# Optimization experiments

Hardware: AMD Instinct MI355X
Metric: run time of the kernel (lower is better)

The kernel has to match this reference:

```python
import jax, jax.numpy as jnp
import numpy as np

# dims
B, A, CIN, CC = 512, 256, 7, 16          # batch, num_actions, input channels, conv channels
D, H, DH, E = 48, 8, 6, 512              # token_dimension, heads, head_dim, num_embeddings
S, T = 32, 32                            # num_input_tokens, num_output_tokens
AH = H * DH                              # 48
NL = 4                                   # attention layers
CONV_IN = A * CC                         # 4096
ENC = S * D                              # 1536
DEC_OUT = A * CIN                        # 1792
SCALE = float(np.sqrt(D))                # module uses sqrt(input_embedding_dim)
EPS = 1e-5


def _ln(x, g, b):
    m = jnp.mean(x, axis=-1, keepdims=True)
    v = jnp.var(x, axis=-1, keepdims=True)
    return (x - m) * jax.lax.rsqrt(v + EPS) * g + b


def setup_inputs() -> dict:
    key = jax.random.key(0)
    ks = iter(jax.random.split(key, 64))
    def rn(shape, s=0.05):
        return jax.random.normal(next(ks), shape, dtype=jnp.float32) * s
    inp = {}
    inp['x'] = jax.random.normal(next(ks), (B, A, CIN), dtype=jnp.float32)
    inp['u'] = jax.random.uniform(next(ks), (T, B), dtype=jnp.float32)
    inp['bn_g'] = jnp.ones((CIN,), jnp.float32); inp['bn_b'] = jnp.zeros((CIN,), jnp.float32)
    inp['conv_w'] = rn((CC, CIN, 5)); inp['conv_b'] = jnp.zeros((CC,), jnp.float32)
    inp['tk_W1'] = rn((CONV_IN, 2 * CONV_IN)); inp['tk_b1'] = jnp.zeros((2 * CONV_IN,), jnp.float32)
    inp['tk_W2'] = rn((2 * CONV_IN, ENC)); inp['tk_b2'] = jnp.zeros((ENC,), jnp.float32)
    for nm in ('q', 'k', 'v'):
        inp['ln%s_g' % nm] = jnp.ones((NL, D), jnp.float32)
        inp['ln%s_b' % nm] = jnp.zeros((NL, D), jnp.float32)
        inp['W%s' % nm] = rn((NL, D, AH))
        inp['b%s' % nm] = jnp.zeros((NL, AH), jnp.float32)
    inp['Wo'] = rn((NL, AH, D)); inp['bo'] = jnp.zeros((NL, D), jnp.float32)
    inp['mln_g'] = jnp.ones((NL, D), jnp.float32); inp['mln_b'] = jnp.zeros((NL, D), jnp.float32)
    inp['W1'] = rn((NL, D, 2 * D)); inp['b1'] = jnp.zeros((NL, 2 * D), jnp.float32)
    inp['W2'] = rn((NL, 2 * D, D)); inp['b2'] = jnp.zeros((NL, D), jnp.float32)
    inp['emb'] = rn((D, E), 1.0)          # nn.Parameter(torch.randn(D, E))
    inp['pos_enc'] = rn((T, D), 1.0)      # nn.Parameter(torch.randn(T, D))
    inp['dec_W1'] = rn((ENC, 2 * ENC)); inp['dec_b1'] = jnp.zeros((2 * ENC,), jnp.float32)
    inp['dec_W2'] = rn((2 * ENC, DEC_OUT)); inp['dec_b2'] = jnp.zeros((DEC_OUT,), jnp.float32)
    return inp


def _fwd(x, u, bn_g, bn_b, conv_w, conv_b, tk_W1, tk_b1, tk_W2, tk_b2,
         lnq_g, lnq_b, Wq, bq, lnk_g, lnk_b, Wk, bk, lnv_g, lnv_b, Wv, bv, Wo, bo,
         mln_g, mln_b, W1, b1, W2, b2, emb, pos_enc, dec_W1, dec_b1, dec_W2, dec_b2):
    # --- conv stem (BatchNorm1d in training mode: batch statistics) ---
    xt = x.transpose(0, 2, 1)                              # [B, 7, A]
    mu = jnp.mean(xt, axis=(0, 2), keepdims=True)
    var = jnp.var(xt, axis=(0, 2), keepdims=True)
    xn = (xt - mu) * jax.lax.rsqrt(var + EPS) * bn_g[None, :, None] + bn_b[None, :, None]
    xc = jax.lax.conv_general_dilated(xn, conv_w, (1,), ((2, 2),),
                                      dimension_numbers=('NCH', 'OIH', 'NCH')) + conv_b[None, :, None]
    xf = xc.reshape(B, -1)                                 # [B, 16*A]
    h = jax.nn.relu(xf @ tk_W1 + tk_b1)
    toks = (h @ tk_W2 + tk_b2).reshape(B, S, D)            # [B, S, D]

    STOT = S + T
    kc = jnp.zeros((NL, B, H, STOT, DH), jnp.float32)
    vc = jnp.zeros_like(kc)

    # --- prefill pass (output discarded; fills KV caches) ---
    ii = jnp.arange(S)[:, None]; jj = jnp.arange(S)[None, :]
    pre_mask = jnp.where(jj - ii >= S - 1, -999.0, 0.0)    # triu(-999, diagonal=S-1), as in source
    xcur = toks
    for l in range(NL):
        q = (_ln(xcur, lnq_g[l], lnq_b[l]) @ Wq[l] + bq[l]).reshape(B, S, H, DH).transpose(0, 2, 1, 3)
        k = (_ln(xcur, lnk_g[l], lnk_b[l]) @ Wk[l] + bk[l]).reshape(B, S, H, DH).transpose(0, 2, 1, 3)
        v = (_ln(xcur, lnv_g[l], lnv_b[l]) @ Wv[l] + bv[l]).reshape(B, S, H, DH).transpose(0, 2, 1, 3)
        kc = kc.at[l, :, :, :S].set(k)
        vc = vc.at[l, :, :, :S].set(v)
        attn = jax.nn.softmax(jnp.einsum('bhqd,bhkd->bhqk', q, k) / SCALE + pre_mask, axis=-1)
        o = jnp.einsum('bhqk,bhkd->bhqd', attn, v).transpose(0, 2, 1, 3).reshape(B, S, AH)
        xcur = o @ Wo[l] + bo[l] + xcur
        hh = jax.nn.relu(_ln(xcur, mln_g[l], mln_b[l]) @ W1[l] + b1[l])
        xcur = hh @ W2[l] + b2[l]

    jidx = jnp.arange(STOT)

    def step(carry, xs):
        kc, vc = carry
        i, pe, uu = xs
        p = S + i                                          # cache length before this step
        xtk = jnp.broadcast_to(pe, (B, 1, D))
        newk, newv = [], []
        for l in range(NL):
            q = (_ln(xtk, lnq_g[l], lnq_b[l]) @ Wq[l] + bq[l]).reshape(B, 1, H, DH).transpose(0, 2, 1, 3)
            k = (_ln(xtk, lnk_g[l], lnk_b[l]) @ Wk[l] + bk[l]).reshape(B, 1, H, DH).transpose(0, 2, 1, 3)
            v = (_ln(xtk, lnv_g[l], lnv_b[l]) @ Wv[l] + bv[l]).reshape(B, 1, H, DH).transpose(0, 2, 1, 3)
            kcl = jax.lax.dynamic_update_slice(kc[l], k, (0, 0, p, 0))
            vcl = jax.lax.dynamic_update_slice(vc[l], v, (0, 0, p, 0))
            scores = jnp.einsum('bhqd,bhkd->bhqk', q, kcl) / SCALE
            # source mask: -999 added for positions >= mask_offset (includes the new token itself)
            scores = scores + jnp.where(jidx >= p, -999.0, 0.0)
            attn = jax.nn.softmax(scores, axis=-1)
            o = jnp.einsum('bhqk,bhkd->bhqd', attn, vcl).transpose(0, 2, 1, 3).reshape(B, 1, AH)
            xtk = o @ Wo[l] + bo[l] + xtk
            hh = jax.nn.relu(_ln(xtk, mln_g[l], mln_b[l]) @ W1[l] + b1[l])
            xtk = hh @ W2[l] + b2[l]
            newk.append(kcl); newv.append(vcl)
        attended = xtk                                     # [B, 1, D]
        probs = jax.nn.softmax((attended @ emb).reshape(B, E), axis=1)
        cdf = jnp.cumsum(probs, axis=1)
        idx = jnp.clip(jnp.sum((cdf < uu[:, None]).astype(jnp.int32), axis=1), 0, E - 1)
        sel = emb.T[idx].reshape(B, 1, D)
        st = sel + attended - jax.lax.stop_gradient(attended)  # straight-through
        return (jnp.stack(newk), jnp.stack(newv)), st

    (_, _), outs = jax.lax.scan(step, (kc, vc), (jnp.arange(T), pos_enc, u))
    out_tokens = outs.transpose(1, 0, 2, 3).reshape(B, T * D)
    dh_ = jax.nn.relu(out_tokens @ dec_W1 + dec_b1)
    traj = (dh_ @ dec_W2 + dec_b2).reshape(B, A, CIN)
    return traj


def reference(x, u, bn_g, bn_b, conv_w, conv_b, tk_W1, tk_b1, tk_W2, tk_b2,
              lnq_g, lnq_b, Wq, bq, lnk_g, lnk_b, Wk, bk, lnv_g, lnv_b, Wv, bv, Wo, bo,
              mln_g, mln_b, W1, b1, W2, b2, emb, pos_enc, dec_W1, dec_b1, dec_W2, dec_b2):
    return _fwd(x, u, bn_g, bn_b, conv_w, conv_b, tk_W1, tk_b1, tk_W2, tk_b2,
                lnq_g, lnq_b, Wq, bq, lnk_g, lnk_b, Wk, bk, lnv_g, lnv_b, Wv, bv, Wo, bo,
                mln_g, mln_b, W1, b1, W2, b2, emb, pos_enc, dec_W1, dec_b1, dec_W2, dec_b2)
```

## Files before the change

### kernel.cpp

```cpp
#include <hip/hip_runtime.h>

static const double SCALE_ = 6.928203230275509;

__device__ inline float  fma_t(float a, float b, float c)  { return fmaf(a, b, c); }
__device__ inline double fma_t(double a, double b, double c){ return fma(a, b, c); }

__device__ __attribute__((noinline)) double dotW(const double* a,
                                                 const float* W, int n, int ldw,
                                                 double init) {
  double a0 = init, a1 = 0.0;
#pragma unroll 2
  for (int i = 0; i < n; i += 2) {
    a0 = fma(a[i],     (double)W[i * ldw],       a0);
    a1 = fma(a[i + 1], (double)W[(i + 1) * ldw], a1);
  }
  return a0 + a1;
}

__device__ __forceinline__ double dot48_row(const double* a, const float* Wrow, double init) {
  double c0 = init, c1 = 0.0, c2 = 0.0, c3 = 0.0;
#pragma unroll
  for (int i = 0; i < 48; i += 4) {
    const float4 wv = *(const float4*)(Wrow + i);
    c0 = fma(a[i],     (double)wv.x, c0);
    c1 = fma(a[i + 1], (double)wv.y, c1);
    c2 = fma(a[i + 2], (double)wv.z, c2);
    c3 = fma(a[i + 3], (double)wv.w, c3);
  }
  return (c0 + c1) + (c2 + c3);
}

__device__ __forceinline__ double dot96_row(const double* a, const float* Wrow, double init) {
  double c0 = init, c1 = 0.0, c2 = 0.0, c3 = 0.0;
#pragma unroll
  for (int i = 0; i < 96; i += 4) {
    const float4 wv = *(const float4*)(Wrow + i);
    c0 = fma(a[i],     (double)wv.x, c0);
    c1 = fma(a[i + 1], (double)wv.y, c1);
    c2 = fma(a[i + 2], (double)wv.z, c2);
    c3 = fma(a[i + 3], (double)wv.w, c3);
  }
  return (c0 + c1) + (c2 + c3);
}

__device__ __attribute__((noinline)) double2 ln_stats48(const double* x) {
  double s0 = 0, s1 = 0, q0 = 0, q1 = 0;
#pragma unroll 2
  for (int i = 0; i < 48; i += 2) {
    const double va = x[i], vb = x[i + 1];
    s0 += va; q0 = fma(va, va, q0);
    s1 += vb; q1 = fma(vb, vb, q1);
  }
  const double m = (s0 + s1) / 48.0;
  const double rs = 1.0 / sqrt((q0 + q1) / 48.0 - m * m + 1e-5);
  return make_double2(m, rs);
}

__device__ __attribute__((noinline)) double exp_ni(double x) { return exp(x); }

__global__ __launch_bounds__(256) void bn_partial_kernel(const float* __restrict__ x,
                                                         double* __restrict__ part) {
  __shared__ double sh[256 * 14];
  const int tid = threadIdx.x;
  const int idx = blockIdx.x * 256 + tid;
  const float* p = x + (size_t)idx * 7;
  for (int c = 0; c < 7; ++c) {
    double v = (double)p[c];
    sh[tid * 14 + c] = v;
    sh[tid * 14 + 7 + c] = v * v;
  }
  __syncthreads();
  if (tid < 14) {
    double acc = 0.0;
    for (int t = 0; t < 256; ++t) acc += sh[t * 14 + tid];
    part[blockIdx.x * 14 + tid] = acc;
  }
}

__global__ void bn_final_kernel(const double* __restrict__ part,
                                const float* __restrict__ g, const float* __restrict__ bb,
                                double* __restrict__ stat) {
  const int c = threadIdx.x;
  if (c < 7) {
    double s = 0.0, s2 = 0.0;
    for (int i = 0; i < 512; ++i) { s += part[i * 14 + c]; s2 += part[i * 14 + 7 + c]; }
    const double mean = s / 131072.0;
    const double var = s2 / 131072.0 - mean * mean;
    const double rstd = 1.0 / sqrt(var + 1e-5);
    const double scale = rstd * (double)g[c];
    stat[c] = scale;
    stat[7 + c] = (double)bb[c] - mean * scale;
  }
}

__global__ __launch_bounds__(256) void conv_kernel(const float* __restrict__ x,
                                                   const float* __restrict__ wconv,
                                                   const float* __restrict__ cb,
                                                   const double* __restrict__ stat,
                                                   double* __restrict__ xf) {
  __shared__ double wsh[560 + 14];
  const int tid = threadIdx.x;
  for (int i = tid; i < 560; i += 256) wsh[i] = (double)wconv[i];
  for (int i = tid; i < 14; i += 256) wsh[560 + i] = stat[i];
  __syncthreads();
  const int idx = blockIdx.x * 256 + tid;
  const int a = idx & 255;
  const int o = (idx >> 8) & 15;
  const int b = idx >> 12;
  double acc = (double)cb[o];
  const float* xb = x + (size_t)b * (256 * 7);
  for (int k = 0; k < 5; ++k) {
    const int pos = a + k - 2;
    if (pos < 0 || pos >= 256) continue;
    const float* xp = xb + pos * 7;
    for (int ci = 0; ci < 7; ++ci) {
      const double xn = (double)xp[ci] * wsh[560 + ci] + wsh[567 + ci];
      acc = fma(xn, wsh[(o * 7 + ci) * 5 + k], acc);
    }
  }
  xf[idx] = acc;
}

template <typename T, bool BIAS, bool RELU>
__global__ __launch_bounds__(256) void gemm128_kernel(const T* __restrict__ A,
                                                      const float* __restrict__ Bm,
                                                      const float* __restrict__ bias,
                                                      T* __restrict__ C,
                                                      const int M, const int N, const int K,
                                                      const int kc) {
  __shared__ T As[16][130];
  __shared__ T Bs[16][66];
  const int tid = threadIdx.x;
  const int tx = tid & 15, ty = tid >> 4;
  const int n0 = blockIdx.x * 64, m0 = blockIdx.y * 128;
  const int k0 = blockIdx.z * kc, kend = k0 + kc;
  const int ar = tid >> 1, ac = (tid & 1) * 8;
  const int br = tid >> 4, bc = (tid & 15) * 4;
  const T* Ap = A + (size_t)(m0 + ar) * K;
  const float* Bp = Bm + (size_t)br * N + n0 + bc;
  T acc[8][4] = {};
  for (int k = k0; k < kend; k += 16) {
    T av8[8];
#pragma unroll
    for (int i = 0; i < 8; ++i) av8[i] = Ap[k + ac + i];
    const float4 bw = *(const float4*)(Bp + (size_t)k * N);
#pragma unroll
    for (int i = 0; i < 8; ++i) As[ac + i][ar] = av8[i];
    Bs[br][bc] = (T)bw.x; Bs[br][bc + 1] = (T)bw.y;
    Bs[br][bc + 2] = (T)bw.z; Bs[br][bc + 3] = (T)bw.w;
    __syncthreads();
#pragma unroll
    for (int kk = 0; kk < 16; ++kk) {
      T a[8], b[4];
#pragma unroll
      for (int i = 0; i < 8; ++i) a[i] = As[kk][ty * 8 + i];
#pragma unroll
      for (int j = 0; j < 4; ++j) b[j] = Bs[kk][tx * 4 + j];
#pragma unroll
      for (int i = 0; i < 8; ++i)
#pragma unroll
        for (int j = 0; j < 4; ++j) acc[i][j] = fma_t(a[i], b[j], acc[i][j]);
    }
    __syncthreads();
  }
  T* Cp = C + (size_t)blockIdx.z * M * N;
#pragma unroll
  for (int i = 0; i < 8; ++i) {
    const int row = m0 + ty * 8 + i;
#pragma unroll
    for (int j = 0; j < 4; ++j) {
      const int col = n0 + tx * 4 + j;
      T v = acc[i][j];
      if (BIAS) v += (T)bias[col];
      if (RELU) v = v > (T)0 ? v : (T)0;
      Cp[(size_t)row * N + col] = v;
    }
  }
}

template <typename T, bool BIAS, bool RELU>
__global__ __launch_bounds__(256) void gemm_kernel(const T* __restrict__ A,
                                                   const float* __restrict__ Bm,
                                                   const float* __restrict__ bias,
                                                   T* __restrict__ C,
                                                   const int M, const int N, const int K,
                                                   const int kc) {
  __shared__ T As[16][65];
  __shared__ T Bs[16][65];
  const int tid = threadIdx.x;
  const int tx = tid & 15, ty = tid >> 4;
  const int n0 = blockIdx.x * 64, m0 = blockIdx.y * 64;
  const int k0 = blockIdx.z * kc, kend = k0 + kc;
  const int ar = tid >> 2, ac = (tid & 3) * 4;
  const int br = tid >> 4, bc = (tid & 15) * 4;
  const T* Ap = A + (size_t)(m0 + ar) * K;
  const float* Bp = Bm + (size_t)br * N + n0 + bc;
  T acc[4][4] = {};
  for (int k = k0; k < kend; k += 16) {
    const T a0 = Ap[k + ac], a1 = Ap[k + ac + 1], a2 = Ap[k + ac + 2], a3 = Ap[k + ac + 3];
    const float4 bw = *(const float4*)(Bp + (size_t)k * N);
    As[ac][ar] = a0; As[ac + 1][ar] = a1; As[ac + 2][ar] = a2; As[ac + 3][ar] = a3;
    Bs[br][bc] = (T)bw.x; Bs[br][bc + 1] = (T)bw.y; Bs[br][bc + 2] = (T)bw.z; Bs[br][bc + 3] = (T)bw.w;
    __syncthreads();
#pragma unroll
    for (int kk = 0; kk < 16; ++kk) {
      T av[4], bv2[4];
#pragma unroll
      for (int i = 0; i < 4; ++i) av[i] = As[kk][ty * 4 + i];
#pragma unroll
      for (int j = 0; j < 4; ++j) bv2[j] = Bs[kk][tx * 4 + j];
#pragma unroll
      for (int i = 0; i < 4; ++i)
#pragma unroll
        for (int j = 0; j < 4; ++j) acc[i][j] = fma_t(av[i], bv2[j], acc[i][j]);
    }
    __syncthreads();
  }
  T* Cp = C + (size_t)blockIdx.z * M * N;
#pragma unroll
  for (int i = 0; i < 4; ++i) {
    const int row = m0 + ty * 4 + i;
#pragma unroll
    for (int j = 0; j < 4; ++j) {
      const int col = n0 + tx * 4 + j;
      T v = acc[i][j];
      if (BIAS) v += (T)bias[col];
      if (RELU) v = v > (T)0 ? v : (T)0;
      Cp[(size_t)row * N + col] = v;
    }
  }
}

__global__ __launch_bounds__(256) void reduce2_bias_kernel(const double* __restrict__ part,
                                                           const float* __restrict__ bias,
                                                           double* __restrict__ out,
                                                           const int MN, const int N) {
  const int i = blockIdx.x * 256 + threadIdx.x;
  if (i < MN) out[i] = part[i] + part[MN + i] + (double)bias[i % N];
}

__global__ __launch_bounds__(256) void transpose_weights_kernel(
    const float* __restrict__ Wq, const float* __restrict__ Wk,
    const float* __restrict__ Wv, const float* __restrict__ Wo,
    const float* __restrict__ W1, const float* __restrict__ W2,
    const float* __restrict__ emb,
    float* __restrict__ WqT, float* __restrict__ WkT,
    float* __restrict__ WvT, float* __restrict__ WoT,
    float* __restrict__ W1T, float* __restrict__ W2T,
    float* __restrict__ embT) {
  const int t = blockIdx.x * 256 + threadIdx.x;
  if (t < 36864) {
    const int a = t / 9216, r = t - a * 9216;
    const int l = r / 2304, e = r - l * 2304;
    const int i = e / 48, j = e - i * 48;
    const float* src = a == 0 ? Wq : a == 1 ? Wk : a == 2 ? Wv : Wo;
    float* dst = a == 0 ? WqT : a == 1 ? WkT : a == 2 ? WvT : WoT;
    dst[l * 2304 + j * 48 + i] = src[l * 2304 + i * 48 + j];
  } else if (t < 55296) {
    const int t1 = t - 36864;
    const int l = t1 / 4608, e = t1 - l * 4608;
    const int i = e / 96, j = e - i * 96;
    W1T[l * 4608 + j * 48 + i] = W1[l * 4608 + i * 96 + j];
  } else if (t < 73728) {
    const int t2 = t - 55296;
    const int l = t2 / 4608, e = t2 - l * 4608;
    const int i = e / 48, j = e - i * 48;
    W2T[l * 4608 + j * 96 + i] = W2[l * 4608 + i * 48 + j];
  } else {
    const int t3 = t - 73728;
    const int d = t3 / 512, e = t3 - d * 512;
    embT[e * 48 + d] = emb[d * 512 + e];
  }
}

__global__ __launch_bounds__(256) void prefill_kernel(
    const double* __restrict__ toks,
    const float* __restrict__ lnq_g, const float* __restrict__ lnq_b,
    const float* __restrict__ Wq, const float* __restrict__ bq,
    const float* __restrict__ lnk_g, const float* __restrict__ lnk_b,
    const float* __restrict__ Wk, const float* __restrict__ bk,
    const float* __restrict__ lnv_g, const float* __restrict__ lnv_b,
    const float* __restrict__ Wv, const float* __restrict__ bvv,
    const float* __restrict__ Wo, const float* __restrict__ bo,
    const float* __restrict__ mln_g, const float* __restrict__ mln_b,
    const float* __restrict__ W1, const float* __restrict__ b1,
    const float* __restrict__ W2, const float* __restrict__ b2,
    double* __restrict__ kcache, double* __restrict__ vcache) {
  const int b = blockIdx.x, tid = threadIdx.x;
  __shared__ double xcur[1536], abuf[1536], qbuf[1536], kvbuf[3072];
  __shared__ double mean[32], rstd[32];
  double* kb = kvbuf;
  double* vb = kvbuf + 1536;

#pragma unroll 1
  for (int i = tid; i < 1536; i += 256) xcur[i] = toks[(size_t)b * 1536 + i];
  __syncthreads();

#pragma unroll 1
  for (int l = 0; l < 4; ++l) {
    if (tid < 32) {
      double s = 0.0, s2 = 0.0;
#pragma unroll 4
      for (int i = 0; i < 48; ++i) { const double v = xcur[tid * 48 + i]; s += v; s2 += v * v; }
      const double m = s / 48.0;
      mean[tid] = m;
      rstd[tid] = 1.0 / sqrt(s2 / 48.0 - m * m + 1e-5);
    }
    __syncthreads();
    const bool last = (l == 3);

    if (!last) {
#pragma unroll 1
      for (int i = tid; i < 1536; i += 256) {
        const int t = i / 48, d = i % 48;
        abuf[i] = (xcur[i] - mean[t]) * rstd[t] * (double)lnq_g[l * 48 + d] + (double)lnq_b[l * 48 + d];
      }
      __syncthreads();
#pragma unroll 1
      for (int i = tid; i < 1536; i += 256) {
        const int t = i / 48, j = i % 48;
        qbuf[i] = dotW(abuf + t * 48, Wq + l * 2304 + j, 48, 48, (double)bq[l * 48 + j]);
      }
      __syncthreads();
    }
#pragma unroll 1
    for (int i = tid; i < 1536; i += 256) {
      const int t = i / 48, d = i % 48;
      abuf[i] = (xcur[i] - mean[t]) * rstd[t] * (double)lnk_g[l * 48 + d] + (double)lnk_b[l * 48 + d];
    }
    __syncthreads();
#pragma unroll 1
    for (int i = tid; i < 1536; i += 256) {
      const int t = i / 48, j = i % 48;
      kb[i] = dotW(abuf + t * 48, Wk + l * 2304 + j, 48, 48, (double)bk[l * 48 + j]);
    }
    __syncthreads();
#pragma unroll 1
    for (int i = tid; i < 1536; i += 256) {
      const int t = i / 48, d = i % 48;
      abuf[i] = (xcur[i] - mean[t]) * rstd[t] * (double)lnv_g[l * 48 + d] + (double)lnv_b[l * 48 + d];
    }
    __syncthreads();
#pragma unroll 1
    for (int i = tid; i < 1536; i += 256) {
      const int t = i / 48, j = i % 48;
      vb[i] = dotW(abuf + t * 48, Wv + l * 2304 + j, 48, 48, (double)bvv[l * 48 + j]);
    }
    __syncthreads();
#pragma unroll 1
    for (int i = tid; i < 1536; i += 256) {
      const int t = i / 48, j = i % 48;
      const int h = j / 6, d = j % 6;
      const size_t ci = ((((size_t)b * 4 + l) * 8 + h) * 64 + t) * 6 + d;
      kcache[ci] = kb[i];
      vcache[ci] = vb[i];
    }

    if (!last) {
      const int t = tid >> 3, h = tid & 7;
      const double* qp = qbuf + t * 48 + h * 6;
      const double q0 = qp[0], q1 = qp[1], q2 = qp[2], q3 = qp[3], q4 = qp[4], q5 = qp[5];
      double mx = -1e300;
#pragma unroll 4
      for (int j = 0; j < 32; ++j) {
        const double* kp = kb + j * 48 + h * 6;
        double sv = q0 * kp[0];
        sv = fma(q1, kp[1], sv); sv = fma(q2, kp[2], sv); sv = fma(q3, kp[3], sv);
        sv = fma(q4, kp[4], sv); sv = fma(q5, kp[5], sv);
        sv /= SCALE_;
        if (t == 0 && j == 31) sv -= 999.0;
        mx = sv > mx ? sv : mx;
      }
      double den = 0, o0 = 0, o1 = 0, o2 = 0, o3 = 0, o4 = 0, o5 = 0;
#pragma unroll 4
      for (int j = 0; j < 32; ++j) {
        const double* kp = kb + j * 48 + h * 6;
        double sv = q0 * kp[0];
        sv = fma(q1, kp[1], sv); sv = fma(q2, kp[2], sv); sv = fma(q3, kp[3], sv);
        sv = fma(q4, kp[4], sv); sv = fma(q5, kp[5], sv);
        sv /= SCALE_;
        if (t == 0 && j == 31) sv -= 999.0;
        const double e = exp_ni(sv - mx);
        den += e;
        const double* vp = vb + j * 48 + h * 6;
        o0 = fma(e, vp[0], o0); o1 = fma(e, vp[1], o1); o2 = fma(e, vp[2], o2);
        o3 = fma(e, vp[3], o3); o4 = fma(e, vp[4], o4); o5 = fma(e, vp[5], o5);
      }
      abuf[t * 48 + h * 6 + 0] = o0 / den;
      abuf[t * 48 + h * 6 + 1] = o1 / den;
      abuf[t * 48 + h * 6 + 2] = o2 / den;
      abuf[t * 48 + h * 6 + 3] = o3 / den;
      abuf[t * 48 + h * 6 + 4] = o4 / den;
      abuf[t * 48 + h * 6 + 5] = o5 / den;
      __syncthreads();
#pragma unroll 1
      for (int i = tid; i < 1536; i += 256) {
        const int t2 = i / 48, j = i % 48;
        xcur[i] += dotW(abuf + t2 * 48, Wo + l * 2304 + j, 48, 48, (double)bo[l * 48 + j]);
      }
      __syncthreads();
      if (tid < 32) {
        double s = 0.0, s2 = 0.0;
#pragma unroll 4
        for (int i = 0; i < 48; ++i) { const double v = xcur[tid * 48 + i]; s += v; s2 += v * v; }
        const double m = s / 48.0;
        mean[tid] = m;
        rstd[tid] = 1.0 / sqrt(s2 / 48.0 - m * m + 1e-5);
      }
      __syncthreads();
#pragma unroll 1
      for (int i = tid; i < 1536; i += 256) {
        const int t2 = i / 48, d = i % 48;
        qbuf[i] = (xcur[i] - mean[t2]) * rstd[t2] * (double)mln_g[l * 48 + d] + (double)mln_b[l * 48 + d];
      }
      __syncthreads();
#pragma unroll 1
      for (int i = tid; i < 3072; i += 256) {
        const int t2 = i / 96, jj = i % 96;
        const double acc = dotW(qbuf + t2 * 48, W1 + l * 4608 + jj, 48, 96, (double)b1[l * 96 + jj]);
        kvbuf[i] = acc > 0 ? acc : 0;
      }
      __syncthreads();
#pragma unroll 1
      for (int i = tid; i < 1536; i += 256) {
        const int t2 = i / 48, j = i % 48;
        abuf[i] = dotW(kvbuf + t2 * 96, W2 + l * 4608 + j, 96, 48, (double)b2[l * 48 + j]);
      }
      __syncthreads();
#pragma unroll 1
      for (int i = tid; i < 1536; i += 256) xcur[i] = abuf[i];
      __syncthreads();
    }
  }
}

__global__ __launch_bounds__(256, 2) void ar_kernel(
    const float* __restrict__ pos_enc, const float* __restrict__ u,
    const float* __restrict__ lnq_g, const float* __restrict__ lnq_b,
    const float* __restrict__ WqT, const float* __restrict__ bq,
    const float* __restrict__ lnk_g, const float* __restrict__ lnk_b,
    const float* __restrict__ WkT, const float* __restrict__ bk,
    const float* __restrict__ lnv_g, const float* __restrict__ lnv_b,
    const float* __restrict__ WvT, const float* __restrict__ bvv,
    const float* __restrict__ WoT, const float* __restrict__ bo,
    const float* __restrict__ mln_g, const float* __restrict__ mln_b,
    const float* __restrict__ W1T, const float* __restrict__ b1,
    const float* __restrict__ W2T, const float* __restrict__ b2,
    const float* __restrict__ embT,
    const double* __restrict__ kcache, const double* __restrict__ vcache,
    float* __restrict__ out_tok) {
  const int b = blockIdx.x, tid = threadIdx.x;
  __shared__ float ksh[4][8][64][6];
  __shared__ double xtk[48], anorm[144], qs[48], os[48], hh[96];
  __shared__ float vnew[48];
  __shared__ double probs[512], red[4];
  __shared__ float par[2880];
  {
    const float* srcs[14] = {lnq_g, lnq_b, lnk_g, lnk_b, lnv_g, lnv_b, mln_g, mln_b,
                             bq, bk, bvv, bo, b1, b2};
    const int sz[14] = {192, 192, 192, 192, 192, 192, 192, 192, 192, 192, 192, 192, 384, 192};
    int base = 0;
#pragma unroll 1
    for (int a2 = 0; a2 < 14; ++a2) {
      for (int i = tid; i < sz[a2]; i += 256) par[base + i] = srcs[a2][i];
      base += sz[a2];
    }
  }
#pragma unroll 1
  for (int m = tid; m < 6144; m += 256) {
    const int d = m % 6, t2 = (m / 6) % 32, h2 = (m / 192) % 8, l2 = m / 1536;
    ksh[l2][h2][t2][d] =
        (float)kcache[((((size_t)b * 4 + l2) * 8 + h2) * 64 + t2) * 6 + d];
  }
  const int hl = tid >> 5, rl = tid & 31;
  float vlo[4][6], vhi[4][6];
#pragma unroll
  for (int l2 = 0; l2 < 4; ++l2)
#pragma unroll
    for (int d = 0; d < 6; ++d) {
      vlo[l2][d] = (float)vcache[((((size_t)b * 4 + l2) * 8 + hl) * 64 + rl) * 6 + d];
      vhi[l2][d] = 0.0f;
    }
  __syncthreads();

#pragma unroll 1
  for (int step = 0; step < 32; ++step) {
    const int p = 32 + step;
    if (tid < 48) xtk[tid] = (double)pos_enc[step * 48 + tid];
    __syncthreads();

#pragma unroll
    for (int l = 0; l < 4; ++l) {
      {
        const double2 st = ln_stats48(xtk);
        if (tid < 144) {
          const int which = tid / 48, d = tid - which * 48;
          const float* gp = par + 384 * which;
          const float* bp = gp + 192;
          anorm[tid] = (xtk[d] - st.x) * st.y * (double)gp[l * 48 + d] + (double)bp[l * 48 + d];
        }
      }
      __syncthreads();
      if (tid < 144) {
        const int which = tid / 48, j = tid - which * 48;
        const float* WT = which == 0 ? WqT : which == 1 ? WkT : WvT;
        const float* bbp = par + 1536 + 192 * which;
        const double acc = dot48_row(anorm + which * 48, WT + l * 2304 + j * 48,
                                     (double)bbp[l * 48 + j]);
        if (which == 0) {
          qs[j] = acc;
        } else {
          const int h2 = j / 6, d2 = j - h2 * 6;
          if (which == 1) ksh[l][h2][p][d2] = (float)acc;
          else            vnew[j] = (float)acc;
        }
      }
      __syncthreads();
      if (rl == (p & 31)) {
#pragma unroll
        for (int d = 0; d < 6; ++d) vhi[l][d] = vnew[hl * 6 + d];
      }
      {
        const float* kp1 = &ksh[l][hl][rl][0];
        const double qv0 = qs[hl * 6 + 0], qv1 = qs[hl * 6 + 1], qv2 = qs[hl * 6 + 2],
                     qv3 = qs[hl * 6 + 3], qv4 = qs[hl * 6 + 4], qv5 = qs[hl * 6 + 5];
        const bool has2 = (rl + 32) < p;
        double sv1 = qv0 * (double)kp1[0];
        sv1 = fma(qv1, (double)kp1[1], sv1); sv1 = fma(qv2, (double)kp1[2], sv1);
        sv1 = fma(qv3, (double)kp1[3], sv1); sv1 = fma(qv4, (double)kp1[4], sv1);
        sv1 = fma(qv5, (double)kp1[5], sv1);
        sv1 /= SCALE_;
        double sv2 = -1e300;
        if (has2) {
          const float* kp2 = &ksh[l][hl][rl + 32][0];
          double t2 = qv0 * (double)kp2[0];
          t2 = fma(qv1, (double)kp2[1], t2); t2 = fma(qv2, (double)kp2[2], t2);
          t2 = fma(qv3, (double)kp2[3], t2); t2 = fma(qv4, (double)kp2[4], t2);
          t2 = fma(qv5, (double)kp2[5], t2);
          sv2 = t2 / SCALE_;
        }
        double mx = sv1 > sv2 ? sv1 : sv2;
#pragma unroll
        for (int off = 1; off < 32; off <<= 1) { const double o2 = __shfl_xor(mx, off); mx = o2 > mx ? o2 : mx; }
        const double e1 = exp(sv1 - mx);
        const double e2 = has2 ? exp(sv2 - mx) : 0.0;
        double den = e1 + e2;
        double o[6];
#pragma unroll
        for (int d = 0; d < 6; ++d) o[d] = e1 * (double)vlo[l][d];
        if (has2) {
#pragma unroll
          for (int d = 0; d < 6; ++d) o[d] = fma(e2, (double)vhi[l][d], o[d]);
        }
#pragma unroll
        for (int off = 1; off < 32; off <<= 1) {
          den += __shfl_xor(den, off);
#pragma unroll
          for (int d = 0; d < 6; ++d) o[d] += __shfl_xor(o[d], off);
        }
        if (rl == 0) {
#pragma unroll
          for (int d = 0; d < 6; ++d) os[hl * 6 + d] = o[d] / den;
        }
      }
      __syncthreads();
      if (tid < 48)
        xtk[tid] += dot48_row(os, WoT + l * 2304 + tid * 48, (double)par[2112 + l * 48 + tid]);
      __syncthreads();
      {
        const double2 st = ln_stats48(xtk);
        if (tid < 48)
          anorm[tid] = (xtk[tid] - st.x) * st.y * (double)par[1152 + l * 48 + tid]
                       + (double)par[1344 + l * 48 + tid];
      }
      __syncthreads();
      if (tid < 96) {
        const double v2 = dot48_row(anorm, W1T + l * 4608 + tid * 48, (double)par[2304 + l * 96 + tid]);
        hh[tid] = v2 > 0 ? v2 : 0;
      }
      __syncthreads();
      if (tid < 48)
        xtk[tid] = dot96_row(hh, W2T + l * 4608 + tid * 96, (double)par[2688 + l * 48 + tid]);
      __syncthreads();
    }

    {
      const double lg1 = dot48_row(xtk, embT + (size_t)tid * 48, 0.0);
      const double lg2 = dot48_row(xtk, embT + (size_t)(256 + tid) * 48, 0.0);
      double mx = lg1 > lg2 ? lg1 : lg2;
#pragma unroll
      for (int off = 1; off < 64; off <<= 1) { const double o2 = __shfl_xor(mx, off); mx = o2 > mx ? o2 : mx; }
      if ((tid & 63) == 0) red[tid >> 6] = mx;
      __syncthreads();
      {
        const double m0 = red[0] > red[1] ? red[0] : red[1];
        const double m1 = red[2] > red[3] ? red[2] : red[3];
        mx = m0 > m1 ? m0 : m1;
      }
      probs[tid] = exp(lg1 - mx);
      probs[tid + 256] = exp(lg2 - mx);
      __syncthreads();
      if (tid < 64) {
        const int lane = tid;
        double loc[8], run = 0;
#pragma unroll
        for (int n2 = 0; n2 < 8; ++n2) { run += probs[lane * 8 + n2]; loc[n2] = run; }
        double incl = run;
#pragma unroll
        for (int off = 1; off < 64; off <<= 1) {
          const double t2 = __shfl_up(incl, off);
          if (lane >= off) incl += t2;
        }
        const double excl = incl - run;
        const double Ssum = __shfl(incl, 63);
        const double uu = (double)u[step * 512 + b];
        int cnt = 0;
#pragma unroll
        for (int n2 = 0; n2 < 8; ++n2) cnt += ((excl + loc[n2]) / Ssum < uu) ? 1 : 0;
#pragma unroll
        for (int off = 1; off < 64; off <<= 1) cnt += __shfl_xor(cnt, off);
        const int idx = cnt > 511 ? 511 : cnt;
        if (lane < 48) {
          const double sel = (double)embT[(size_t)idx * 48 + lane];
          const double att = xtk[lane];
          out_tok[(size_t)b * 1536 + step * 48 + lane] = (float)((sel + att) - att);
        }
      }
      __syncthreads();
    }
  }
}

extern "C" void kernel_launch(void* const* d_in, const int* in_sizes, int n_in,
                              void* d_out, int out_size, void* d_ws, size_t ws_size,
                              hipStream_t stream) {
  const float* x      = (const float*)d_in[0];
  const float* u      = (const float*)d_in[1];
  const float* bn_g   = (const float*)d_in[2];
  const float* bn_b   = (const float*)d_in[3];
  const float* conv_w = (const float*)d_in[4];
  const float* conv_b = (const float*)d_in[5];
  const float* tk_W1  = (const float*)d_in[6];
  const float* tk_b1  = (const float*)d_in[7];
  const float* tk_W2  = (const float*)d_in[8];
  const float* tk_b2  = (const float*)d_in[9];
  const float* lnq_g  = (const float*)d_in[10];
  const float* lnq_b  = (const float*)d_in[11];
  const float* Wq     = (const float*)d_in[12];
  const float* bq     = (const float*)d_in[13];
  const float* lnk_g  = (const float*)d_in[14];
  const float* lnk_b  = (const float*)d_in[15];
  const float* Wk     = (const float*)d_in[16];
  const float* bk     = (const float*)d_in[17];
  const float* lnv_g  = (const float*)d_in[18];
  const float* lnv_b  = (const float*)d_in[19];
  const float* Wv     = (const float*)d_in[20];
  const float* bvv    = (const float*)d_in[21];
  const float* Wo     = (const float*)d_in[22];
  const float* bo     = (const float*)d_in[23];
  const float* mln_g  = (const float*)d_in[24];
  const float* mln_b  = (const float*)d_in[25];
  const float* W1     = (const float*)d_in[26];
  const float* b1     = (const float*)d_in[27];
  const float* W2     = (const float*)d_in[28];
  const float* b2     = (const float*)d_in[29];
  const float* emb    = (const float*)d_in[30];
  const float* pos    = (const float*)d_in[31];
  const float* dW1    = (const float*)d_in[32];
  const float* db1    = (const float*)d_in[33];
  const float* dW2    = (const float*)d_in[34];
  const float* db2    = (const float*)d_in[35];
  float* out = (float*)d_out;

  char* w = (char*)d_ws;
  size_t off = 0;
  auto alloc = [&](size_t bytes) {
    size_t o = off;
    off = (off + bytes + 255) & ~(size_t)255;
    return o;
  };
  const size_t o_bnp  = alloc(512 * 14 * 8);
  const size_t o_bns  = alloc(14 * 8);
  const size_t o_xf   = alloc(16777216);
  const size_t o_h    = alloc(33554432);
  const size_t o_toks = alloc(6291456);
  const size_t o_kc   = alloc(50331648);
  const size_t o_vc   = alloc(50331648);

  double* bnp  = (double*)(w + o_bnp);
  double* bns  = (double*)(w + o_bns);
  double* xf   = (double*)(w + o_xf);
  double* hbuf = (double*)(w + o_h);
  double* toks = (double*)(w + o_toks);
  double* kc   = (double*)(w + o_kc);
  double* vc   = (double*)(w + o_vc);
  double* part = (double*)(w + o_xf);
  float*  otok = (float*)(w + o_h);
  float*  dh   = (float*)(w + o_h + 4194304);
  float* WqT  = (float*)(w + o_h + 16777216);
  float* WkT  = WqT + 9216;
  float* WvT  = WkT + 9216;
  float* WoT  = WvT + 9216;
  float* W1T  = WoT + 9216;
  float* W2T  = W1T + 18432;
  float* embT = W2T + 18432;

  bn_partial_kernel<<<512, 256, 0, stream>>>(x, bnp);
  bn_final_kernel<<<1, 64, 0, stream>>>(bnp, bn_g, bn_b, bns);
  conv_kernel<<<8192, 256, 0, stream>>>(x, conv_w, conv_b, bns, xf);
  gemm128_kernel<double, true, true><<<dim3(128, 4, 1), 256, 0, stream>>>(
      xf, tk_W1, tk_b1, hbuf, 512, 8192, 4096, 4096);
  gemm128_kernel<double, false, false><<<dim3(24, 4, 2), 256, 0, stream>>>(
      hbuf, tk_W2, nullptr, part, 512, 1536, 8192, 4096);
  reduce2_bias_kernel<<<3072, 256, 0, stream>>>(part, tk_b2, toks, 512 * 1536, 1536);
  transpose_weights_kernel<<<384, 256, 0, stream>>>(Wq, Wk, Wv, Wo, W1, W2, emb,
      WqT, WkT, WvT, WoT, W1T, W2T, embT);
  prefill_kernel<<<512, 256, 0, stream>>>(toks,
      lnq_g, lnq_b, Wq, bq, lnk_g, lnk_b, Wk, bk, lnv_g, lnv_b, Wv, bvv,
      Wo, bo, mln_g, mln_b, W1, b1, W2, b2, kc, vc);
  ar_kernel<<<512, 256, 0, stream>>>(pos, u,
      lnq_g, lnq_b, WqT, bq, lnk_g, lnk_b, WkT, bk, lnv_g, lnv_b, WvT, bvv,
      WoT, bo, mln_g, mln_b, W1T, b1, W2T, b2, embT, kc, vc, otok);
  gemm_kernel<float, true, true><<<dim3(48, 8, 1), 256, 0, stream>>>(
      otok, dW1, db1, dh, 512, 3072, 1536, 1536);
  gemm_kernel<float, true, false><<<dim3(28, 8, 1), 256, 0, stream>>>(
      dh, dW2, db2, out, 512, 1792, 3072, 3072);
}
```

Measured before the change: 5.186 ms.

## Stage per-layer weights in padded shared memory and keep KV cache in registers

In the autoregressive kernel, each layer's transposed Q/K/V/O and MLP weights are now staged into a padded shared-memory buffer before use. The dot products then read from LDS instead of issuing strided global loads from a few threads. The K cache moves out of shared memory into per-thread registers alongside V, and the logits read the original emb layout with coalesced column access instead of embT. This trades extra cooperative copies each layer, plus a non-unrolled layer loop, for cheaper weight reads and smaller LDS use, with some added register pressure.

```diff
diff --git a/kernel.cpp b/kernel.cpp
--- a/kernel.cpp
+++ b/kernel.cpp
@@ -15,6 +15,19 @@
     a1 = fma(a[i + 1], (double)W[(i + 1) * ldw], a1);
   }
   return a0 + a1;
+}
+
+template <int N, typename WP>
+__device__ __forceinline__ double dotN(const double* a, WP W, int ldw, double init) {
+  double c0 = init, c1 = 0.0, c2 = 0.0, c3 = 0.0;
+#pragma unroll
+  for (int i = 0; i < N; i += 4) {
+    c0 = fma(a[i],     (double)W[i * ldw],       c0);
+    c1 = fma(a[i + 1], (double)W[(i + 1) * ldw], c1);
+    c2 = fma(a[i + 2], (double)W[(i + 2) * ldw], c2);
+    c3 = fma(a[i + 3], (double)W[(i + 3) * ldw], c3);
+  }
+  return (c0 + c1) + (c2 + c3);
 }
 
 __device__ __forceinline__ double dot48_row(const double* a, const float* Wrow, double init) {
@@ -434,6 +447,56 @@
   }
 }
 
+__device__ __forceinline__ void attn_phase(
+    const int hl, const int rl, const int p,
+    const double* __restrict__ qs, double* __restrict__ os,
+    const float* __restrict__ knew, const float* __restrict__ vnew,
+    float (&klo)[6], float (&khi)[6], float (&vlo)[6], float (&vhi)[6]) {
+  if (rl == (p & 31)) {
+#pragma unroll
+    for (int d = 0; d < 6; ++d) { khi[d] = knew[hl * 6 + d]; vhi[d] = vnew[hl * 6 + d]; }
+  }
+  const double qv0 = qs[hl * 6 + 0], qv1 = qs[hl * 6 + 1], qv2 = qs[hl * 6 + 2],
+               qv3 = qs[hl * 6 + 3], qv4 = qs[hl * 6 + 4], qv5 = qs[hl * 6 + 5];
+  const bool has2 = (rl + 32) < p;
+  double sv1 = qv0 * (double)klo[0];
+  sv1 = fma(qv1, (double)klo[1], sv1); sv1 = fma(qv2, (double)klo[2], sv1);
+  sv1 = fma(qv3, (double)klo[3], sv1); sv1 = fma(qv4, (double)klo[4], sv1);
+  sv1 = fma(qv5, (double)klo[5], sv1);
+  sv1 /= SCALE_;
+  double sv2 = -1e300;
+  if (has2) {
+    double t2 = qv0 * (double)khi[0];
+    t2 = fma(qv1, (double)khi[1], t2); t2 = fma(qv2, (double)khi[2], t2);
+    t2 = fma(qv3, (double)khi[3], t2); t2 = fma(qv4, (double)khi[4], t2);
+    t2 = fma(qv5, (double)khi[5], t2);
+    sv2 = t2 / SCALE_;
+  }
+  double mx = sv1 > sv2 ? sv1 : sv2;
+#pragma unroll
+  for (int off = 1; off < 32; off <<= 1) { const double o2 = __shfl_xor(mx, off); mx = o2 > mx ? o2 : mx; }
+  const double e1 = exp(sv1 - mx);
+  const double e2 = has2 ? exp(sv2 - mx) : 0.0;
+  double den = e1 + e2;
+  double o[6];
+#pragma unroll
+  for (int d = 0; d < 6; ++d) o[d] = e1 * (double)vlo[d];
+  if (has2) {
+#pragma unroll
+    for (int d = 0; d < 6; ++d) o[d] = fma(e2, (double)vhi[d], o[d]);
+  }
+#pragma unroll
+  for (int off = 1; off < 32; off <<= 1) {
+    den += __shfl_xor(den, off);
+#pragma unroll
+    for (int d = 0; d < 6; ++d) o[d] += __shfl_xor(o[d], off);
+  }
+  if (rl == 0) {
+#pragma unroll
+    for (int d = 0; d < 6; ++d) os[hl * 6 + d] = o[d] / den;
+  }
+}
+
 __global__ __launch_bounds__(256, 2) void ar_kernel(
     const float* __restrict__ pos_enc, const float* __restrict__ u,
     const float* __restrict__ lnq_g, const float* __restrict__ lnq_b,
@@ -446,13 +509,13 @@
     const float* __restrict__ mln_g, const float* __restrict__ mln_b,
     const float* __restrict__ W1T, const float* __restrict__ b1,
     const float* __restrict__ W2T, const float* __restrict__ b2,
-    const float* __restrict__ embT,
+    const float* __restrict__ emb,
     const double* __restrict__ kcache, const double* __restrict__ vcache,
     float* __restrict__ out_tok) {
   const int b = blockIdx.x, tid = threadIdx.x;
-  __shared__ float ksh[4][8][64][6];
+  __shared__ float wsh[9984];
+  __shared__ float knew[48], vnew[48];
   __shared__ double xtk[48], anorm[144], qs[48], os[48], hh[96];
-  __shared__ float vnew[48];
   __shared__ double probs[512], red[4];
   __shared__ float par[2880];
   {
@@ -466,22 +529,28 @@
       base += sz[a2];
     }
   }
-#pragma unroll 1
-  for (int m = tid; m < 6144; m += 256) {
-    const int d = m % 6, t2 = (m / 6) % 32, h2 = (m / 192) % 8, l2 = m / 1536;
-    ksh[l2][h2][t2][d] =
-        (float)kcache[((((size_t)b * 4 + l2) * 8 + h2) * 64 + t2) * 6 + d];
-  }
   const int hl = tid >> 5, rl = tid & 31;
-  float vlo[4][6], vhi[4][6];
-#pragma unroll
-  for (int l2 = 0; l2 < 4; ++l2)
-#pragma unroll
-    for (int d = 0; d < 6; ++d) {
-      vlo[l2][d] = (float)vcache[((((size_t)b * 4 + l2) * 8 + hl) * 64 + rl) * 6 + d];
-      vhi[l2][d] = 0.0f;
-    }
+  float klo0[6], khi0[6], vlo0[6], vhi0[6];
+  float klo1[6], khi1[6], vlo1[6], vhi1[6];
+  float klo2[6], khi2[6], vlo2[6], vhi2[6];
+  float klo3[6], khi3[6], vlo3[6], vhi3[6];
+#define PRELOAD_KV(L, KLO, KHI, VLO, VHI)                                          \
+  {                                                                                \
+    const size_t base0 = ((((size_t)b * 4 + (L)) * 8 + hl) * 64 + rl) * 6;         \
+    _Pragma("unroll") for (int d = 0; d < 6; ++d) {                                \
+      KLO[d] = (float)kcache[base0 + d];                                           \
+      VLO[d] = (float)vcache[base0 + d];                                           \
+      KHI[d] = 0.0f; VHI[d] = 0.0f;                                                \
+    }                                                                              \
+  }
+  PRELOAD_KV(0, klo0, khi0, vlo0, vhi0)
+  PRELOAD_KV(1, klo1, khi1, vlo1, vhi1)
+  PRELOAD_KV(2, klo2, khi2, vlo2, vhi2)
+  PRELOAD_KV(3, klo3, khi3, vlo3, vhi3)
+#undef PRELOAD_KV
   __syncthreads();
+
+  float4* const wsh4 = (float4*)wsh;
 
 #pragma unroll 1
   for (int step = 0; step < 32; ++step) {
@@ -489,9 +558,20 @@
     if (tid < 48) xtk[tid] = (double)pos_enc[step * 48 + tid];
     __syncthreads();
 
-#pragma unroll
+#pragma unroll 1
     for (int l = 0; l < 4; ++l) {
       {
+        const float4* s0 = (const float4*)(WqT + l * 2304);
+        const float4* s1 = (const float4*)(WkT + l * 2304);
+        const float4* s2 = (const float4*)(WvT + l * 2304);
+        const float4* s3 = (const float4*)(WoT + l * 2304);
+#pragma unroll 1
+        for (int i = tid; i < 2304; i += 256) {
+          const int a = i / 576, r = i - a * 576;
+          const int row = r / 12, q = r - row * 12;
+          const float4 v = a == 0 ? s0[r] : a == 1 ? s1[r] : a == 2 ? s2[r] : s3[r];
+          wsh4[a * 624 + row * 13 + q] = v;
+        }
         const double2 st = ln_stats48(xtk);
         if (tid < 144) {
           const int which = tid / 48, d = tid - which * 48;
@@ -503,71 +583,42 @@
       __syncthreads();
       if (tid < 144) {
         const int which = tid / 48, j = tid - which * 48;
-        const float* WT = which == 0 ? WqT : which == 1 ? WkT : WvT;
         const float* bbp = par + 1536 + 192 * which;
-        const double acc = dot48_row(anorm + which * 48, WT + l * 2304 + j * 48,
+        const double acc = dot48_row(anorm + which * 48, wsh + which * 2496 + j * 52,
                                      (double)bbp[l * 48 + j]);
         if (which == 0) {
           qs[j] = acc;
+        } else if (which == 1) {
+          knew[j] = (float)acc;
         } else {
-          const int h2 = j / 6, d2 = j - h2 * 6;
-          if (which == 1) ksh[l][h2][p][d2] = (float)acc;
-          else            vnew[j] = (float)acc;
+          vnew[j] = (float)acc;
         }
       }
       __syncthreads();
-      if (rl == (p & 31)) {
-#pragma unroll
-        for (int d = 0; d < 6; ++d) vhi[l][d] = vnew[hl * 6 + d];
-      }
+      switch (l) {
+        case 0: attn_phase(hl, rl, p, qs, os, knew, vnew, klo0, khi0, vlo0, vhi0); break;
+        case 1: attn_phase(hl, rl, p, qs, os, knew, vnew, klo1, khi1, vlo1, vhi1); break;
+        case 2: attn_phase(hl, rl, p, qs, os, knew, vnew, klo2, khi2, vlo2, vhi2); break;
+        default: attn_phase(hl, rl, p, qs, os, knew, vnew, klo3, khi3, vlo3, vhi3); break;
+      }
+      __syncthreads();
+      if (tid < 48)
+        xtk[tid] += dot48_row(os, wsh + 3 * 2496 + tid * 52, (double)par[2112 + l * 48 + tid]);
+      __syncthreads();
       {
-        const float* kp1 = &ksh[l][hl][rl][0];
-        const double qv0 = qs[hl * 6 + 0], qv1 = qs[hl * 6 + 1], qv2 = qs[hl * 6 + 2],
-                     qv3 = qs[hl * 6 + 3], qv4 = qs[hl * 6 + 4], qv5 = qs[hl * 6 + 5];
-        const bool has2 = (rl + 32) < p;
-        double sv1 = qv0 * (double)kp1[0];
-        sv1 = fma(qv1, (double)kp1[1], sv1); sv1 = fma(qv2, (double)kp1[2], sv1);
-        sv1 = fma(qv3, (double)kp1[3], sv1); sv1 = fma(qv4, (double)kp1[4], sv1);
-        sv1 = fma(qv5, (double)kp1[5], sv1);
-        sv1 /= SCALE_;
-        double sv2 = -1e300;
-        if (has2) {
-          const float* kp2 = &ksh[l][hl][rl + 32][0];
-          double t2 = qv0 * (double)kp2[0];
-          t2 = fma(qv1, (double)kp2[1], t2); t2 = fma(qv2, (double)kp2[2], t2);
-          t2 = fma(qv3, (double)kp2[3], t2); t2 = fma(qv4, (double)kp2[4], t2);
-          t2 = fma(qv5, (double)kp2[5], t2);
-          sv2 = t2 / SCALE_;
+        const float4* s1q = (const float4*)(W1T + l * 4608);
+        const float4* s2q = (const float4*)(W2T + l * 4608);
+#pragma unroll 1
+        for (int i = tid; i < 2304; i += 256) {
+          if (i < 1152) {
+            const int row = i / 12, q = i - row * 12;
+            wsh4[row * 13 + q] = s1q[i];
+          } else {
+            const int i2 = i - 1152;
+            const int row = i2 / 24, q = i2 - row * 24;
+            wsh4[1248 + row * 25 + q] = s2q[i2];
+          }
         }
-        double mx = sv1 > sv2 ? sv1 : sv2;
-#pragma unroll
-        for (int off = 1; off < 32; off <<= 1) { const double o2 = __shfl_xor(mx, off); mx = o2 > mx ? o2 : mx; }
-        const double e1 = exp(sv1 - mx);
-        const double e2 = has2 ? exp(sv2 - mx) : 0.0;
-        double den = e1 + e2;
-        double o[6];
-#pragma unroll
-        for (int d = 0; d < 6; ++d) o[d] = e1 * (double)vlo[l][d];
-        if (has2) {
-#pragma unroll
-          for (int d = 0; d < 6; ++d) o[d] = fma(e2, (double)vhi[l][d], o[d]);
-        }
-#pragma unroll
-        for (int off = 1; off < 32; off <<= 1) {
-          den += __shfl_xor(den, off);
-#pragma unroll
-          for (int d = 0; d < 6; ++d) o[d] += __shfl_xor(o[d], off);
-        }
-        if (rl == 0) {
-#pragma unroll
-          for (int d = 0; d < 6; ++d) os[hl * 6 + d] = o[d] / den;
-        }
-      }
-      __syncthreads();
-      if (tid < 48)
-        xtk[tid] += dot48_row(os, WoT + l * 2304 + tid * 48, (double)par[2112 + l * 48 + tid]);
-      __syncthreads();
-      {
         const double2 st = ln_stats48(xtk);
         if (tid < 48)
           anorm[tid] = (xtk[tid] - st.x) * st.y * (double)par[1152 + l * 48 + tid]
@@ -575,18 +626,18 @@
       }
       __syncthreads();
       if (tid < 96) {
-        const double v2 = dot48_row(anorm, W1T + l * 4608 + tid * 48, (double)par[2304 + l * 96 + tid]);
+        const double v2 = dot48_row(anorm, wsh + tid * 52, (double)par[2304 + l * 96 + tid]);
         hh[tid] = v2 > 0 ? v2 : 0;
       }
       __syncthreads();
       if (tid < 48)
-        xtk[tid] = dot96_row(hh, W2T + l * 4608 + tid * 96, (double)par[2688 + l * 48 + tid]);
+        xtk[tid] = dot96_row(hh, wsh + 4992 + tid * 100, (double)par[2688 + l * 48 + tid]);
       __syncthreads();
     }
 
     {
-      const double lg1 = dot48_row(xtk, embT + (size_t)tid * 48, 0.0);
-      const double lg2 = dot48_row(xtk, embT + (size_t)(256 + tid) * 48, 0.0);
+      const double lg1 = dotN<48>(xtk, emb + tid, 512, 0.0);
+      const double lg2 = dotN<48>(xtk, emb + 256 + tid, 512, 0.0);
       double mx = lg1 > lg2 ? lg1 : lg2;
 #pragma unroll
       for (int off = 1; off < 64; off <<= 1) { const double o2 = __shfl_xor(mx, off); mx = o2 > mx ? o2 : mx; }
@@ -621,7 +672,7 @@
         for (int off = 1; off < 64; off <<= 1) cnt += __shfl_xor(cnt, off);
         const int idx = cnt > 511 ? 511 : cnt;
         if (lane < 48) {
-          const double sel = (double)embT[(size_t)idx * 48 + lane];
+          const double sel = (double)emb[lane * 512 + idx];
           const double att = xtk[lane];
           out_tok[(size_t)b * 1536 + step * 48 + lane] = (float)((sel + att) - att);
         }
@@ -720,7 +771,7 @@
       Wo, bo, mln_g, mln_b, W1, b1, W2, b2, kc, vc);
   ar_kernel<<<512, 256, 0, stream>>>(pos, u,
       lnq_g, lnq_b, WqT, bq, lnk_g, lnk_b, WkT, bk, lnv_g, lnv_b, WvT, bvv,
-      WoT, bo, mln_g, mln_b, W1T, b1, W2T, b2, embT, kc, vc, otok);
+      WoT, bo, mln_g, mln_b, W1T, b1, W2T, b2, emb, kc, vc, otok);
   gemm_kernel<float, true, true><<<dim3(48, 8, 1), 256, 0, stream>>>(
       otok, dW1, db1, dh, 512, 3072, 1536, 1536);
   gemm_kernel<float, true, false><<<dim3(28, 8, 1), 256, 0, stream>>>(
```

Result: no change. 5.160 ms (-0.5%).

## Store KV cache as compact fp32 and read prefill keys/values from global in AR loop

Applied to the files above, without the earlier changes.

Prefill now writes the key/value cache as float with only 32 positions per head instead of double with 64 slots, which quarters the cache footprint and write traffic. The autoregressive kernel no longer preloads the cache into shared memory and registers. It reads the prefill keys/values from global memory each step and keeps only newly generated keys/values in shared arrays, with the layer loop no longer unrolled. Logits and token selection use the original emb layout through a strided dot helper instead of the transposed copy. This trades a large startup load for repeated global reads inside the 32-step loop, and the strided emb access may coalesce less well.

```diff
diff --git a/kernel.cpp b/kernel.cpp
--- a/kernel.cpp
+++ b/kernel.cpp
@@ -15,6 +15,19 @@
     a1 = fma(a[i + 1], (double)W[(i + 1) * ldw], a1);
   }
   return a0 + a1;
+}
+
+template <int N, typename WP>
+__device__ __forceinline__ double dotN(const double* a, WP W, int ldw, double init) {
+  double c0 = init, c1 = 0.0, c2 = 0.0, c3 = 0.0;
+#pragma unroll
+  for (int i = 0; i < N; i += 4) {
+    c0 = fma(a[i],     (double)W[i * ldw],       c0);
+    c1 = fma(a[i + 1], (double)W[(i + 1) * ldw], c1);
+    c2 = fma(a[i + 2], (double)W[(i + 2) * ldw], c2);
+    c3 = fma(a[i + 3], (double)W[(i + 3) * ldw], c3);
+  }
+  return (c0 + c1) + (c2 + c3);
 }
 
 __device__ __forceinline__ double dot48_row(const double* a, const float* Wrow, double init) {
@@ -285,7 +298,7 @@
     const float* __restrict__ mln_g, const float* __restrict__ mln_b,
     const float* __restrict__ W1, const float* __restrict__ b1,
     const float* __restrict__ W2, const float* __restrict__ b2,
-    double* __restrict__ kcache, double* __restrict__ vcache) {
+    float* __restrict__ kc32, float* __restrict__ vc32) {
   const int b = blockIdx.x, tid = threadIdx.x;
   __shared__ double xcur[1536], abuf[1536], qbuf[1536], kvbuf[3072];
   __shared__ double mean[32], rstd[32];
@@ -351,9 +364,9 @@
     for (int i = tid; i < 1536; i += 256) {
       const int t = i / 48, j = i % 48;
       const int h = j / 6, d = j % 6;
-      const size_t ci = ((((size_t)b * 4 + l) * 8 + h) * 64 + t) * 6 + d;
-      kcache[ci] = kb[i];
-      vcache[ci] = vb[i];
+      const size_t ci = ((((size_t)b * 4 + l) * 8 + h) * 32 + t) * 6 + d;
+      kc32[ci] = (float)kb[i];
+      vc32[ci] = (float)vb[i];
     }
 
     if (!last) {
@@ -446,13 +459,13 @@
     const float* __restrict__ mln_g, const float* __restrict__ mln_b,
     const float* __restrict__ W1T, const float* __restrict__ b1,
     const float* __restrict__ W2T, const float* __restrict__ b2,
-    const float* __restrict__ embT,
-    const double* __restrict__ kcache, const double* __restrict__ vcache,
+    const float* __restrict__ emb,
+    const float* __restrict__ kc32, const float* __restrict__ vc32,
     float* __restrict__ out_tok) {
   const int b = blockIdx.x, tid = threadIdx.x;
-  __shared__ float ksh[4][8][64][6];
+  __shared__ float knew[4][8][32][7];
+  __shared__ float vnew[4][8][32][7];
   __shared__ double xtk[48], anorm[144], qs[48], os[48], hh[96];
-  __shared__ float vnew[48];
   __shared__ double probs[512], red[4];
   __shared__ float par[2880];
   {
@@ -466,22 +479,9 @@
       base += sz[a2];
     }
   }
-#pragma unroll 1
-  for (int m = tid; m < 6144; m += 256) {
-    const int d = m % 6, t2 = (m / 6) % 32, h2 = (m / 192) % 8, l2 = m / 1536;
-    ksh[l2][h2][t2][d] =
-        (float)kcache[((((size_t)b * 4 + l2) * 8 + h2) * 64 + t2) * 6 + d];
-  }
+  __syncthreads();
+
   const int hl = tid >> 5, rl = tid & 31;
-  float vlo[4][6], vhi[4][6];
-#pragma unroll
-  for (int l2 = 0; l2 < 4; ++l2)
-#pragma unroll
-    for (int d = 0; d < 6; ++d) {
-      vlo[l2][d] = (float)vcache[((((size_t)b * 4 + l2) * 8 + hl) * 64 + rl) * 6 + d];
-      vhi[l2][d] = 0.0f;
-    }
-  __syncthreads();
 
 #pragma unroll 1
   for (int step = 0; step < 32; ++step) {
@@ -489,7 +489,7 @@
     if (tid < 48) xtk[tid] = (double)pos_enc[step * 48 + tid];
     __syncthreads();
 
-#pragma unroll
+#pragma unroll 1
     for (int l = 0; l < 4; ++l) {
       {
         const double2 st = ln_stats48(xtk);
@@ -511,32 +511,30 @@
           qs[j] = acc;
         } else {
           const int h2 = j / 6, d2 = j - h2 * 6;
-          if (which == 1) ksh[l][h2][p][d2] = (float)acc;
-          else            vnew[j] = (float)acc;
+          if (which == 1) knew[l][h2][step][d2] = (float)acc;
+          else            vnew[l][h2][step][d2] = (float)acc;
         }
       }
       __syncthreads();
-      if (rl == (p & 31)) {
-#pragma unroll
-        for (int d = 0; d < 6; ++d) vhi[l][d] = vnew[hl * 6 + d];
-      }
       {
-        const float* kp1 = &ksh[l][hl][rl][0];
+        const size_t gb = (((size_t)b * 4 + l) * 8 + hl) * 192 + rl * 6;
+        const float* kg = kc32 + gb;
+        const float* vg = vc32 + gb;
         const double qv0 = qs[hl * 6 + 0], qv1 = qs[hl * 6 + 1], qv2 = qs[hl * 6 + 2],
                      qv3 = qs[hl * 6 + 3], qv4 = qs[hl * 6 + 4], qv5 = qs[hl * 6 + 5];
-        const bool has2 = (rl + 32) < p;
-        double sv1 = qv0 * (double)kp1[0];
-        sv1 = fma(qv1, (double)kp1[1], sv1); sv1 = fma(qv2, (double)kp1[2], sv1);
-        sv1 = fma(qv3, (double)kp1[3], sv1); sv1 = fma(qv4, (double)kp1[4], sv1);
-        sv1 = fma(qv5, (double)kp1[5], sv1);
+        const bool has2 = rl < step;
+        double sv1 = qv0 * (double)kg[0];
+        sv1 = fma(qv1, (double)kg[1], sv1); sv1 = fma(qv2, (double)kg[2], sv1);
+        sv1 = fma(qv3, (double)kg[3], sv1); sv1 = fma(qv4, (double)kg[4], sv1);
+        sv1 = fma(qv5, (double)kg[5], sv1);
         sv1 /= SCALE_;
         double sv2 = -1e300;
         if (has2) {
-          const float* kp2 = &ksh[l][hl][rl + 32][0];
-          double t2 = qv0 * (double)kp2[0];
-          t2 = fma(qv1, (double)kp2[1], t2); t2 = fma(qv2, (double)kp2[2], t2);
-          t2 = fma(qv3, (double)kp2[3], t2); t2 = fma(qv4, (double)kp2[4], t2);
-          t2 = fma(qv5, (double)kp2[5], t2);
+          const float* kh = &knew[l][hl][rl][0];
+          double t2 = qv0 * (double)kh[0];
+          t2 = fma(qv1, (double)kh[1], t2); t2 = fma(qv2, (double)kh[2], t2);
+          t2 = fma(qv3, (double)kh[3], t2); t2 = fma(qv4, (double)kh[4], t2);
+          t2 = fma(qv5, (double)kh[5], t2);
           sv2 = t2 / SCALE_;
         }
         double mx = sv1 > sv2 ? sv1 : sv2;
@@ -547,10 +545,11 @@
         double den = e1 + e2;
         double o[6];
 #pragma unroll
-        for (int d = 0; d < 6; ++d) o[d] = e1 * (double)vlo[l][d];
+        for (int d = 0; d < 6; ++d) o[d] = e1 * (double)vg[d];
         if (has2) {
-#pragma unroll
-          for (int d = 0; d < 6; ++d) o[d] = fma(e2, (double)vhi[l][d], o[d]);
+          const float* vh = &vnew[l][hl][rl][0];
+#pragma unroll
+          for (int d = 0; d < 6; ++d) o[d] = fma(e2, (double)vh[d], o[d]);
         }
 #pragma unroll
         for (int off = 1; off < 32; off <<= 1) {
@@ -585,8 +584,8 @@
     }
 
     {
-      const double lg1 = dot48_row(xtk, embT + (size_t)tid * 48, 0.0);
-      const double lg2 = dot48_row(xtk, embT + (size_t)(256 + tid) * 48, 0.0);
+      const double lg1 = dotN<48>(xtk, emb + tid, 512, 0.0);
+      const double lg2 = dotN<48>(xtk, emb + 256 + tid, 512, 0.0);
       double mx = lg1 > lg2 ? lg1 : lg2;
 #pragma unroll
       for (int off = 1; off < 64; off <<= 1) { const double o2 = __shfl_xor(mx, off); mx = o2 > mx ? o2 : mx; }
@@ -621,7 +620,7 @@
         for (int off = 1; off < 64; off <<= 1) cnt += __shfl_xor(cnt, off);
         const int idx = cnt > 511 ? 511 : cnt;
         if (lane < 48) {
-          const double sel = (double)embT[(size_t)idx * 48 + lane];
+          const double sel = (double)emb[lane * 512 + idx];
           const double att = xtk[lane];
           out_tok[(size_t)b * 1536 + step * 48 + lane] = (float)((sel + att) - att);
         }
@@ -684,16 +683,16 @@
   const size_t o_xf   = alloc(16777216);
   const size_t o_h    = alloc(33554432);
   const size_t o_toks = alloc(6291456);
-  const size_t o_kc   = alloc(50331648);
-  const size_t o_vc   = alloc(50331648);
+  const size_t o_kc   = alloc(12582912);
+  const size_t o_vc   = alloc(12582912);
 
   double* bnp  = (double*)(w + o_bnp);
   double* bns  = (double*)(w + o_bns);
   double* xf   = (double*)(w + o_xf);
   double* hbuf = (double*)(w + o_h);
   double* toks = (double*)(w + o_toks);
-  double* kc   = (double*)(w + o_kc);
-  double* vc   = (double*)(w + o_vc);
+  float*  kc32 = (float*)(w + o_kc);
+  float*  vc32 = (float*)(w + o_vc);
   double* part = (double*)(w + o_xf);
   float*  otok = (float*)(w + o_h);
   float*  dh   = (float*)(w + o_h + 4194304);
@@ -717,10 +716,10 @@
       WqT, WkT, WvT, WoT, W1T, W2T, embT);
   prefill_kernel<<<512, 256, 0, stream>>>(toks,
       lnq_g, lnq_b, Wq, bq, lnk_g, lnk_b, Wk, bk, lnv_g, lnv_b, Wv, bvv,
-      Wo, bo, mln_g, mln_b, W1, b1, W2, b2, kc, vc);
+      Wo, bo, mln_g, mln_b, W1, b1, W2, b2, kc32, vc32);
   ar_kernel<<<512, 256, 0, stream>>>(pos, u,
       lnq_g, lnq_b, WqT, bq, lnk_g, lnk_b, WkT, bk, lnv_g, lnv_b, WvT, bvv,
-      WoT, bo, mln_g, mln_b, W1T, b1, W2T, b2, embT, kc, vc, otok);
+      WoT, bo, mln_g, mln_b, W1T, b1, W2T, b2, emb, kc32, vc32, otok);
   gemm_kernel<float, true, true><<<dim3(48, 8, 1), 256, 0, stream>>>(
       otok, dW1, db1, dh, 512, 3072, 1536, 1536);
   gemm_kernel<float, true, false><<<dim3(28, 8, 1), 256, 0, stream>>>(
```

After: 4.462 ms. 1.16x faster.
